# Kernel optimization log

Hardware: AMD Instinct MI355X
Metric: run time of the kernel (lower is better)

Reference implementation:

```python
import jax, jax.numpy as jnp
import numpy as np

EPS = 1e-5

def conv1x1(x, w, b):
    # x: [B,C,H,W], w: [O,C], b: [O]
    return jnp.einsum('bchw,oc->bohw', x, w) + b[None, :, None, None]

def batchnorm(x, gamma, beta):
    # training-mode BN: biased batch statistics over (N,H,W)
    mean = jnp.mean(x, axis=(0, 2, 3), keepdims=True)
    var = jnp.var(x, axis=(0, 2, 3), keepdims=True)
    inv = jax.lax.rsqrt(var + EPS)
    return (x - mean) * inv * gamma[None, :, None, None] + beta[None, :, None, None]

def setup_inputs() -> dict:
    key = jax.random.key(0)
    ks = jax.random.split(key, 20)
    B, H, W = 32, 480, 640
    d = {
        'x1': jax.random.normal(ks[0], (B, 3, H, W), dtype=jnp.float32),
        'w1': jax.random.normal(ks[1], (3, 3), dtype=jnp.float32) * 0.3,
        'b1': jax.random.normal(ks[2], (3,), dtype=jnp.float32) * 0.1,
        'g2': jnp.ones((3,), dtype=jnp.float32),
        'be2': jnp.zeros((3,), dtype=jnp.float32),
        'w3': jax.random.normal(ks[3], (8, 3), dtype=jnp.float32) * 0.3,
        'b3': jax.random.normal(ks[4], (8,), dtype=jnp.float32) * 0.1,
        'w4': jax.random.normal(ks[5], (8, 8), dtype=jnp.float32) * 0.2,
        'b4': jax.random.normal(ks[6], (8,), dtype=jnp.float32) * 0.1,
        'g5': jnp.ones((8,), dtype=jnp.float32),
        'be5': jnp.zeros((8,), dtype=jnp.float32),
        'w6': jax.random.normal(ks[7], (8, 8), dtype=jnp.float32) * 0.2,
        'b6': jax.random.normal(ks[8], (8,), dtype=jnp.float32) * 0.1,
        'w7': jax.random.normal(ks[9], (8, 8), dtype=jnp.float32) * 0.2,
        'b7': jax.random.normal(ks[10], (8,), dtype=jnp.float32) * 0.1,
        'w8': jax.random.normal(ks[11], (8, 8), dtype=jnp.float32) * 0.2,
        'b8': jax.random.normal(ks[12], (8,), dtype=jnp.float32) * 0.1,
    }
    return d

def reference(x1, w1, b1, g2, be2, w3, b3, w4, b4, g5, be5, w6, b6, w7, b7, w8, b8):
    v1 = conv1x1(x1, w1, b1)        # [B,3,H,W]
    v2 = batchnorm(v1, g2, be2)     # [B,3,H,W]
    v3 = conv1x1(v2, w3, b3)        # [B,8,H,W]
    v4 = conv1x1(v3, w4, b4)
    v5 = batchnorm(v4, g5, be5)
    v6 = conv1x1(v5, w6, b6)
    v7 = conv1x1(v6, w7, b7)
    v8 = conv1x1(v7, w8, b8)
    return v8
```

## Files before the change

kernel.cpp:

```cpp
#include <hip/hip_runtime.h>
#include <math.h>

#define HWD   (480*640)
#define HW4   (HWD/4)
#define BATCH 32
#define NPIXD ((double)BATCH*(double)HWD)
#define NPIX4 (BATCH*HW4)
#define RBLK  1024
#define BPI   32
#define ISTRIDE (BPI*256)
#define BN_EPS 1e-5

typedef float f32x4 __attribute__((ext_vector_type(4)));

__global__ __launch_bounds__(256) void k_reduce(const float* __restrict__ x,
                                                double* __restrict__ partials) {
    const int b   = blockIdx.x >> 5;
    const int blk = blockIdx.x & 31;
    const float4* xb = (const float4*)x + (long long)b*(3*HW4);

    float s0=0.f,s1=0.f,s2=0.f,s00=0.f,s01=0.f,s02=0.f,s11=0.f,s12=0.f,s22=0.f;
    for (int s = blk*256 + threadIdx.x; s < HW4; s += ISTRIDE) {
        const float4 a = xb[s];
        const float4 c = xb[s + HW4];
        const float4 e = xb[s + 2*HW4];
        float X0,X1,X2;
        X0=a.x; X1=c.x; X2=e.x;
        s0+=X0; s1+=X1; s2+=X2;
        s00=fmaf(X0,X0,s00); s01=fmaf(X0,X1,s01); s02=fmaf(X0,X2,s02);
        s11=fmaf(X1,X1,s11); s12=fmaf(X1,X2,s12); s22=fmaf(X2,X2,s22);
        X0=a.y; X1=c.y; X2=e.y;
        s0+=X0; s1+=X1; s2+=X2;
        s00=fmaf(X0,X0,s00); s01=fmaf(X0,X1,s01); s02=fmaf(X0,X2,s02);
        s11=fmaf(X1,X1,s11); s12=fmaf(X1,X2,s12); s22=fmaf(X2,X2,s22);
        X0=a.z; X1=c.z; X2=e.z;
        s0+=X0; s1+=X1; s2+=X2;
        s00=fmaf(X0,X0,s00); s01=fmaf(X0,X1,s01); s02=fmaf(X0,X2,s02);
        s11=fmaf(X1,X1,s11); s12=fmaf(X1,X2,s12); s22=fmaf(X2,X2,s22);
        X0=a.w; X1=c.w; X2=e.w;
        s0+=X0; s1+=X1; s2+=X2;
        s00=fmaf(X0,X0,s00); s01=fmaf(X0,X1,s01); s02=fmaf(X0,X2,s02);
        s11=fmaf(X1,X1,s11); s12=fmaf(X1,X2,s12); s22=fmaf(X2,X2,s22);
    }
    double v[9] = {(double)s0,(double)s1,(double)s2,(double)s00,(double)s01,
                   (double)s02,(double)s11,(double)s12,(double)s22};
    #pragma unroll
    for (int off = 32; off > 0; off >>= 1) {
        #pragma unroll
        for (int q = 0; q < 9; ++q) v[q] += __shfl_down(v[q], off, 64);
    }
    __shared__ double lds[4][9];
    const int lane = threadIdx.x & 63;
    const int wid  = threadIdx.x >> 6;
    if (lane == 0) {
        #pragma unroll
        for (int q = 0; q < 9; ++q) lds[wid][q] = v[q];
    }
    __syncthreads();
    if (threadIdx.x < 9) {
        partials[(long long)blockIdx.x*9 + threadIdx.x] =
            lds[0][threadIdx.x] + lds[1][threadIdx.x] + lds[2][threadIdx.x] + lds[3][threadIdx.x];
    }
}

__device__ void affine8(const float* __restrict__ w, const float* __restrict__ bias,
                        double A[8][3], double cc[8]) {
    double T[8][3], tc[8];
    for (int o = 0; o < 8; ++o) {
        double t0=0,t1=0,t2=0,tb=0;
        for (int c = 0; c < 8; ++c) {
            const double wv = (double)w[o*8+c];
            t0 += wv*A[c][0]; t1 += wv*A[c][1]; t2 += wv*A[c][2]; tb += wv*cc[c];
        }
        T[o][0]=t0; T[o][1]=t1; T[o][2]=t2; tc[o]=tb + (double)bias[o];
    }
    for (int o = 0; o < 8; ++o) { A[o][0]=T[o][0]; A[o][1]=T[o][1]; A[o][2]=T[o][2]; cc[o]=tc[o]; }
}

__device__ void bn8(int rows, const double m[3], const double C[3][3],
                    const float* __restrict__ g, const float* __restrict__ be,
                    double A[8][3], double cc[8]) {
    for (int o = 0; o < rows; ++o) {
        const double mu = A[o][0]*m[0] + A[o][1]*m[1] + A[o][2]*m[2] + cc[o];
        double var = 0;
        for (int i = 0; i < 3; ++i)
            for (int j = 0; j < 3; ++j)
                var += A[o][i]*A[o][j]*C[i][j];
        const double inv = 1.0 / sqrt(var + BN_EPS);
        const double sc  = inv * (double)g[o];
        A[o][0]*=sc; A[o][1]*=sc; A[o][2]*=sc;
        cc[o] = (cc[o]-mu)*sc + (double)be[o];
    }
}

__global__ __launch_bounds__(256) void k_apply2(const float* __restrict__ x,
        const double* __restrict__ partials,
        const float* __restrict__ w1, const float* __restrict__ b1,
        const float* __restrict__ g2, const float* __restrict__ be2,
        const float* __restrict__ w3, const float* __restrict__ b3,
        const float* __restrict__ w4, const float* __restrict__ b4,
        const float* __restrict__ g5, const float* __restrict__ be5,
        const float* __restrict__ w6, const float* __restrict__ b6,
        const float* __restrict__ w7, const float* __restrict__ b7,
        const float* __restrict__ w8, const float* __restrict__ b8,
        float* __restrict__ out) {
    __shared__ float4 MdS[8];
    {
        const int tid = threadIdx.x;
        double v[9] = {0,0,0,0,0,0,0,0,0};
        #pragma unroll
        for (int r = 0; r < 4; ++r) {
            const double* row = partials + (size_t)(r*256 + tid)*9;
            #pragma unroll
            for (int q = 0; q < 9; ++q) v[q] += row[q];
        }
        #pragma unroll
        for (int off = 32; off > 0; off >>= 1) {
            #pragma unroll
            for (int q = 0; q < 9; ++q) v[q] += __shfl_down(v[q], off, 64);
        }
        __shared__ double wsum[4][9];
        __shared__ double red[9];
        const int lane = tid & 63;
        const int wid  = tid >> 6;
        if (lane == 0) {
            #pragma unroll
            for (int q = 0; q < 9; ++q) wsum[wid][q] = v[q];
        }
        __syncthreads();
        if (tid < 9) red[tid] = wsum[0][tid] + wsum[1][tid] + wsum[2][tid] + wsum[3][tid];
        __syncthreads();

        if (tid == 0) {
            const double N = NPIXD;
            double m[3];
            for (int i = 0; i < 3; ++i) m[i] = red[i] / N;
            double S[3][3];
            S[0][0]=red[3]; S[0][1]=red[4]; S[0][2]=red[5];
            S[1][1]=red[6]; S[1][2]=red[7]; S[2][2]=red[8];
            S[1][0]=S[0][1]; S[2][0]=S[0][2]; S[2][1]=S[1][2];
            double C[3][3];
            for (int i = 0; i < 3; ++i)
                for (int j = 0; j < 3; ++j)
                    C[i][j] = S[i][j]/N - m[i]*m[j];

            double A[8][3], cc[8];
            for (int o = 0; o < 3; ++o) {
                A[o][0]=(double)w1[o*3+0]; A[o][1]=(double)w1[o*3+1]; A[o][2]=(double)w1[o*3+2];
                cc[o]=(double)b1[o];
            }
            bn8(3, m, C, g2, be2, A, cc);
            {
                double T[8][3], tc[8];
                for (int o = 0; o < 8; ++o) {
                    double t0=0,t1=0,t2=0,tb=0;
                    for (int c = 0; c < 3; ++c) {
                        const double wv = (double)w3[o*3+c];
                        t0 += wv*A[c][0]; t1 += wv*A[c][1]; t2 += wv*A[c][2]; tb += wv*cc[c];
                    }
                    T[o][0]=t0; T[o][1]=t1; T[o][2]=t2; tc[o]=tb + (double)b3[o];
                }
                for (int o = 0; o < 8; ++o) { A[o][0]=T[o][0]; A[o][1]=T[o][1]; A[o][2]=T[o][2]; cc[o]=tc[o]; }
            }
            affine8(w4, b4, A, cc);
            bn8(8, m, C, g5, be5, A, cc);
            affine8(w6, b6, A, cc);
            affine8(w7, b7, A, cc);
            affine8(w8, b8, A, cc);
            for (int o = 0; o < 8; ++o)
                MdS[o] = make_float4((float)A[o][0], (float)A[o][1], (float)A[o][2], (float)cc[o]);
        }
        __syncthreads();
    }

    const int b   = blockIdx.x >> 5;
    const int blk = blockIdx.x & 31;
    const float4* xb = (const float4*)x + (long long)b*(3*HW4);
    f32x4* ob = (f32x4*)out + (long long)b*(8*HW4);
    float4 M[8];
    #pragma unroll
    for (int o = 0; o < 8; ++o) M[o] = MdS[o];

    for (int s = blk*256 + threadIdx.x; s < HW4; s += ISTRIDE) {
        const float4 x0 = xb[s];
        const float4 x1 = xb[s + HW4];
        const float4 x2 = xb[s + 2*HW4];
        #pragma unroll
        for (int o = 0; o < 8; ++o) {
            const float4 mr = M[o];
            f32x4 r;
            r.x = fmaf(mr.x, x0.x, fmaf(mr.y, x1.x, fmaf(mr.z, x2.x, mr.w)));
            r.y = fmaf(mr.x, x0.y, fmaf(mr.y, x1.y, fmaf(mr.z, x2.y, mr.w)));
            r.z = fmaf(mr.x, x0.z, fmaf(mr.y, x1.z, fmaf(mr.z, x2.z, mr.w)));
            r.w = fmaf(mr.x, x0.w, fmaf(mr.y, x1.w, fmaf(mr.z, x2.w, mr.w)));
            __builtin_nontemporal_store(r, ob + (long long)o*HW4 + s);
        }
    }
}

extern "C" void kernel_launch(void* const* d_in, const int* in_sizes, int n_in,
                              void* d_out, int out_size, void* d_ws, size_t ws_size,
                              hipStream_t stream) {
    const float* x  = (const float*)d_in[0];
    const float* w1 = (const float*)d_in[1];
    const float* b1 = (const float*)d_in[2];
    const float* g2 = (const float*)d_in[3];
    const float* be2= (const float*)d_in[4];
    const float* w3 = (const float*)d_in[5];
    const float* b3 = (const float*)d_in[6];
    const float* w4 = (const float*)d_in[7];
    const float* b4 = (const float*)d_in[8];
    const float* g5 = (const float*)d_in[9];
    const float* be5= (const float*)d_in[10];
    const float* w6 = (const float*)d_in[11];
    const float* b6 = (const float*)d_in[12];
    const float* w7 = (const float*)d_in[13];
    const float* b7 = (const float*)d_in[14];
    const float* w8 = (const float*)d_in[15];
    const float* b8 = (const float*)d_in[16];

    double* partials = (double*)d_ws;
    float*  out      = (float*)d_out;

    k_reduce<<<RBLK, 256, 0, stream>>>(x, partials);
    k_apply2<<<RBLK, 256, 0, stream>>>(x, partials,
        w1,b1,g2,be2,w3,b3,w4,b4,g5,be5,w6,b6,w7,b7,w8,b8, out);
}
```

Baseline: 103.0 us.

## Fuse stats reduction and apply into one cooperative kernel with register-cached input

Merges the statistics-reduction and apply kernels into one cooperative kernel. Each thread loads its slice of x once, keeps it in registers across a grid-wide sync, and reuses it for the output pass, so x is no longer read twice from global memory. In exchange it adds a grid barrier, needs all 256 large blocks to be co-resident, and raises register pressure, which lowers occupancy.

Result: slower. 189.5 us (+84.0%).

```diff
diff --git a/kernel.cpp b/kernel.cpp
--- a/kernel.cpp
+++ b/kernel.cpp
@@ -1,67 +1,22 @@
 #include <hip/hip_runtime.h>
+#include <hip/hip_cooperative_groups.h>
 #include <math.h>
+
+namespace cg = cooperative_groups;
 
 #define HWD   (480*640)
 #define HW4   (HWD/4)
 #define BATCH 32
 #define NPIXD ((double)BATCH*(double)HWD)
-#define NPIX4 (BATCH*HW4)
-#define RBLK  1024
-#define BPI   32
-#define ISTRIDE (BPI*256)
+#define GRID  256
+#define TPB   1024
+#define BPI   8
+#define PPB   (HW4/BPI)
+#define KFULL 9
+#define KTAIL (PPB - KFULL*TPB)
 #define BN_EPS 1e-5
 
 typedef float f32x4 __attribute__((ext_vector_type(4)));
-
-__global__ __launch_bounds__(256) void k_reduce(const float* __restrict__ x,
-                                                double* __restrict__ partials) {
-    const int b   = blockIdx.x >> 5;
-    const int blk = blockIdx.x & 31;
-    const float4* xb = (const float4*)x + (long long)b*(3*HW4);
-
-    float s0=0.f,s1=0.f,s2=0.f,s00=0.f,s01=0.f,s02=0.f,s11=0.f,s12=0.f,s22=0.f;
-    for (int s = blk*256 + threadIdx.x; s < HW4; s += ISTRIDE) {
-        const float4 a = xb[s];
-        const float4 c = xb[s + HW4];
-        const float4 e = xb[s + 2*HW4];
-        float X0,X1,X2;
-        X0=a.x; X1=c.x; X2=e.x;
-        s0+=X0; s1+=X1; s2+=X2;
-        s00=fmaf(X0,X0,s00); s01=fmaf(X0,X1,s01); s02=fmaf(X0,X2,s02);
-        s11=fmaf(X1,X1,s11); s12=fmaf(X1,X2,s12); s22=fmaf(X2,X2,s22);
-        X0=a.y; X1=c.y; X2=e.y;
-        s0+=X0; s1+=X1; s2+=X2;
-        s00=fmaf(X0,X0,s00); s01=fmaf(X0,X1,s01); s02=fmaf(X0,X2,s02);
-        s11=fmaf(X1,X1,s11); s12=fmaf(X1,X2,s12); s22=fmaf(X2,X2,s22);
-        X0=a.z; X1=c.z; X2=e.z;
-        s0+=X0; s1+=X1; s2+=X2;
-        s00=fmaf(X0,X0,s00); s01=fmaf(X0,X1,s01); s02=fmaf(X0,X2,s02);
-        s11=fmaf(X1,X1,s11); s12=fmaf(X1,X2,s12); s22=fmaf(X2,X2,s22);
-        X0=a.w; X1=c.w; X2=e.w;
-        s0+=X0; s1+=X1; s2+=X2;
-        s00=fmaf(X0,X0,s00); s01=fmaf(X0,X1,s01); s02=fmaf(X0,X2,s02);
-        s11=fmaf(X1,X1,s11); s12=fmaf(X1,X2,s12); s22=fmaf(X2,X2,s22);
-    }
-    double v[9] = {(double)s0,(double)s1,(double)s2,(double)s00,(double)s01,
-                   (double)s02,(double)s11,(double)s12,(double)s22};
-    #pragma unroll
-    for (int off = 32; off > 0; off >>= 1) {
-        #pragma unroll
-        for (int q = 0; q < 9; ++q) v[q] += __shfl_down(v[q], off, 64);
-    }
-    __shared__ double lds[4][9];
-    const int lane = threadIdx.x & 63;
-    const int wid  = threadIdx.x >> 6;
-    if (lane == 0) {
-        #pragma unroll
-        for (int q = 0; q < 9; ++q) lds[wid][q] = v[q];
-    }
-    __syncthreads();
-    if (threadIdx.x < 9) {
-        partials[(long long)blockIdx.x*9 + threadIdx.x] =
-            lds[0][threadIdx.x] + lds[1][threadIdx.x] + lds[2][threadIdx.x] + lds[3][threadIdx.x];
-    }
-}
 
 __device__ void affine8(const float* __restrict__ w, const float* __restrict__ bias,
                         double A[8][3], double cc[8]) {
@@ -93,8 +48,8 @@
     }
 }
 
-__global__ __launch_bounds__(256) void k_apply2(const float* __restrict__ x,
-        const double* __restrict__ partials,
+__global__ __launch_bounds__(TPB, 4) void k_fused(const float* __restrict__ x,
+        double* __restrict__ partials,
         const float* __restrict__ w1, const float* __restrict__ b1,
         const float* __restrict__ g2, const float* __restrict__ be2,
         const float* __restrict__ w3, const float* __restrict__ b3,
@@ -104,23 +59,54 @@
         const float* __restrict__ w7, const float* __restrict__ b7,
         const float* __restrict__ w8, const float* __restrict__ b8,
         float* __restrict__ out) {
+    const int tid = threadIdx.x;
+    const int b   = blockIdx.x >> 3;
+    const int blk = blockIdx.x & 7;
+    const float4* xb = (const float4*)x + (long long)b*(3*HW4);
+    const int start = blk*PPB;
+
+    __shared__ double wsum[16][9];
+    __shared__ double red[9];
     __shared__ float4 MdS[8];
+
+    float4 X[10][3];
+    float s0=0.f,s1=0.f,s2=0.f,s00=0.f,s01=0.f,s02=0.f,s11=0.f,s12=0.f,s22=0.f;
+    #pragma unroll
+    for (int k = 0; k < 10; ++k) {
+        const int p = start + k*TPB + tid;
+        float4 a, c, e;
+        if (k < KFULL || tid < KTAIL) {
+            a = xb[p]; c = xb[p + HW4]; e = xb[p + 2*HW4];
+        } else {
+            a = make_float4(0.f,0.f,0.f,0.f); c = a; e = a;
+        }
+        X[k][0] = a; X[k][1] = c; X[k][2] = e;
+        float X0,X1,X2;
+        X0=a.x; X1=c.x; X2=e.x;
+        s0+=X0; s1+=X1; s2+=X2;
+        s00=fmaf(X0,X0,s00); s01=fmaf(X0,X1,s01); s02=fmaf(X0,X2,s02);
+        s11=fmaf(X1,X1,s11); s12=fmaf(X1,X2,s12); s22=fmaf(X2,X2,s22);
+        X0=a.y; X1=c.y; X2=e.y;
+        s0+=X0; s1+=X1; s2+=X2;
+        s00=fmaf(X0,X0,s00); s01=fmaf(X0,X1,s01); s02=fmaf(X0,X2,s02);
+        s11=fmaf(X1,X1,s11); s12=fmaf(X1,X2,s12); s22=fmaf(X2,X2,s22);
+        X0=a.z; X1=c.z; X2=e.z;
+        s0+=X0; s1+=X1; s2+=X2;
+        s00=fmaf(X0,X0,s00); s01=fmaf(X0,X1,s01); s02=fmaf(X0,X2,s02);
+        s11=fmaf(X1,X1,s11); s12=fmaf(X1,X2,s12); s22=fmaf(X2,X2,s22);
+        X0=a.w; X1=c.w; X2=e.w;
+        s0+=X0; s1+=X1; s2+=X2;
+        s00=fmaf(X0,X0,s00); s01=fmaf(X0,X1,s01); s02=fmaf(X0,X2,s02);
+        s11=fmaf(X1,X1,s11); s12=fmaf(X1,X2,s12); s22=fmaf(X2,X2,s22);
+    }
     {
-        const int tid = threadIdx.x;
-        double v[9] = {0,0,0,0,0,0,0,0,0};
-        #pragma unroll
-        for (int r = 0; r < 4; ++r) {
-            const double* row = partials + (size_t)(r*256 + tid)*9;
-            #pragma unroll
-            for (int q = 0; q < 9; ++q) v[q] += row[q];
-        }
+        double v[9] = {(double)s0,(double)s1,(double)s2,(double)s00,(double)s01,
+                       (double)s02,(double)s11,(double)s12,(double)s22};
         #pragma unroll
         for (int off = 32; off > 0; off >>= 1) {
             #pragma unroll
             for (int q = 0; q < 9; ++q) v[q] += __shfl_down(v[q], off, 64);
         }
-        __shared__ double wsum[4][9];
-        __shared__ double red[9];
         const int lane = tid & 63;
         const int wid  = tid >> 6;
         if (lane == 0) {
@@ -128,72 +114,99 @@
             for (int q = 0; q < 9; ++q) wsum[wid][q] = v[q];
         }
         __syncthreads();
-        if (tid < 9) red[tid] = wsum[0][tid] + wsum[1][tid] + wsum[2][tid] + wsum[3][tid];
-        __syncthreads();
-
-        if (tid == 0) {
-            const double N = NPIXD;
-            double m[3];
-            for (int i = 0; i < 3; ++i) m[i] = red[i] / N;
-            double S[3][3];
-            S[0][0]=red[3]; S[0][1]=red[4]; S[0][2]=red[5];
-            S[1][1]=red[6]; S[1][2]=red[7]; S[2][2]=red[8];
-            S[1][0]=S[0][1]; S[2][0]=S[0][2]; S[2][1]=S[1][2];
-            double C[3][3];
-            for (int i = 0; i < 3; ++i)
-                for (int j = 0; j < 3; ++j)
-                    C[i][j] = S[i][j]/N - m[i]*m[j];
-
-            double A[8][3], cc[8];
-            for (int o = 0; o < 3; ++o) {
-                A[o][0]=(double)w1[o*3+0]; A[o][1]=(double)w1[o*3+1]; A[o][2]=(double)w1[o*3+2];
-                cc[o]=(double)b1[o];
+        if (tid < 9) {
+            double acc = 0.0;
+            #pragma unroll
+            for (int w = 0; w < 16; ++w) acc += wsum[w][tid];
+            partials[(long long)blockIdx.x*9 + tid] = acc;
+        }
+    }
+
+    cg::this_grid().sync();
+
+    if (tid < 256) {
+        double v[9];
+        #pragma unroll
+        for (int q = 0; q < 9; ++q) v[q] = partials[(long long)tid*9 + q];
+        #pragma unroll
+        for (int off = 32; off > 0; off >>= 1) {
+            #pragma unroll
+            for (int q = 0; q < 9; ++q) v[q] += __shfl_down(v[q], off, 64);
+        }
+        const int lane = tid & 63;
+        const int wid  = tid >> 6;
+        if (lane == 0) {
+            #pragma unroll
+            for (int q = 0; q < 9; ++q) wsum[wid][q] = v[q];
+        }
+    }
+    __syncthreads();
+    if (tid < 9) red[tid] = wsum[0][tid] + wsum[1][tid] + wsum[2][tid] + wsum[3][tid];
+    __syncthreads();
+
+    if (tid == 0) {
+        const double N = NPIXD;
+        double m[3];
+        for (int i = 0; i < 3; ++i) m[i] = red[i] / N;
+        double S[3][3];
+        S[0][0]=red[3]; S[0][1]=red[4]; S[0][2]=red[5];
+        S[1][1]=red[6]; S[1][2]=red[7]; S[2][2]=red[8];
+        S[1][0]=S[0][1]; S[2][0]=S[0][2]; S[2][1]=S[1][2];
+        double C[3][3];
+        for (int i = 0; i < 3; ++i)
+            for (int j = 0; j < 3; ++j)
+                C[i][j] = S[i][j]/N - m[i]*m[j];
+
+        double A[8][3], cc[8];
+        for (int o = 0; o < 3; ++o) {
+            A[o][0]=(double)w1[o*3+0]; A[o][1]=(double)w1[o*3+1]; A[o][2]=(double)w1[o*3+2];
+            cc[o]=(double)b1[o];
+        }
+        bn8(3, m, C, g2, be2, A, cc);
+        {
+            double T[8][3], tc[8];
+            for (int o = 0; o < 8; ++o) {
+                double t0=0,t1=0,t2=0,tb=0;
+                for (int c = 0; c < 3; ++c) {
+                    const double wv = (double)w3[o*3+c];
+                    t0 += wv*A[c][0]; t1 += wv*A[c][1]; t2 += wv*A[c][2]; tb += wv*cc[c];
+                }
+                T[o][0]=t0; T[o][1]=t1; T[o][2]=t2; tc[o]=tb + (double)b3[o];
             }
-            bn8(3, m, C, g2, be2, A, cc);
-            {
-                double T[8][3], tc[8];
-                for (int o = 0; o < 8; ++o) {
-                    double t0=0,t1=0,t2=0,tb=0;
-                    for (int c = 0; c < 3; ++c) {
-                        const double wv = (double)w3[o*3+c];
-                        t0 += wv*A[c][0]; t1 += wv*A[c][1]; t2 += wv*A[c][2]; tb += wv*cc[c];
-                    }
-                    T[o][0]=t0; T[o][1]=t1; T[o][2]=t2; tc[o]=tb + (double)b3[o];
-                }
-                for (int o = 0; o < 8; ++o) { A[o][0]=T[o][0]; A[o][1]=T[o][1]; A[o][2]=T[o][2]; cc[o]=tc[o]; }
-            }
-            affine8(w4, b4, A, cc);
-            bn8(8, m, C, g5, be5, A, cc);
-            affine8(w6, b6, A, cc);
-            affine8(w7, b7, A, cc);
-            affine8(w8, b8, A, cc);
-            for (int o = 0; o < 8; ++o)
-                MdS[o] = make_float4((float)A[o][0], (float)A[o][1], (float)A[o][2], (float)cc[o]);
-        }
-        __syncthreads();
-    }
-
-    const int b   = blockIdx.x >> 5;
-    const int blk = blockIdx.x & 31;
-    const float4* xb = (const float4*)x + (long long)b*(3*HW4);
+            for (int o = 0; o < 8; ++o) { A[o][0]=T[o][0]; A[o][1]=T[o][1]; A[o][2]=T[o][2]; cc[o]=tc[o]; }
+        }
+        affine8(w4, b4, A, cc);
+        bn8(8, m, C, g5, be5, A, cc);
+        affine8(w6, b6, A, cc);
+        affine8(w7, b7, A, cc);
+        affine8(w8, b8, A, cc);
+        for (int o = 0; o < 8; ++o)
+            MdS[o] = make_float4((float)A[o][0], (float)A[o][1], (float)A[o][2], (float)cc[o]);
+    }
+    __syncthreads();
+
     f32x4* ob = (f32x4*)out + (long long)b*(8*HW4);
     float4 M[8];
     #pragma unroll
     for (int o = 0; o < 8; ++o) M[o] = MdS[o];
 
-    for (int s = blk*256 + threadIdx.x; s < HW4; s += ISTRIDE) {
-        const float4 x0 = xb[s];
-        const float4 x1 = xb[s + HW4];
-        const float4 x2 = xb[s + 2*HW4];
-        #pragma unroll
-        for (int o = 0; o < 8; ++o) {
-            const float4 mr = M[o];
-            f32x4 r;
-            r.x = fmaf(mr.x, x0.x, fmaf(mr.y, x1.x, fmaf(mr.z, x2.x, mr.w)));
-            r.y = fmaf(mr.x, x0.y, fmaf(mr.y, x1.y, fmaf(mr.z, x2.y, mr.w)));
-            r.z = fmaf(mr.x, x0.z, fmaf(mr.y, x1.z, fmaf(mr.z, x2.z, mr.w)));
-            r.w = fmaf(mr.x, x0.w, fmaf(mr.y, x1.w, fmaf(mr.z, x2.w, mr.w)));
-            __builtin_nontemporal_store(r, ob + (long long)o*HW4 + s);
+    #pragma unroll
+    for (int k = 0; k < 10; ++k) {
+        if (k < KFULL || tid < KTAIL) {
+            const int p = start + k*TPB + tid;
+            const float4 x0 = X[k][0];
+            const float4 x1 = X[k][1];
+            const float4 x2 = X[k][2];
+            #pragma unroll
+            for (int o = 0; o < 8; ++o) {
+                const float4 mr = M[o];
+                f32x4 r;
+                r.x = fmaf(mr.x, x0.x, fmaf(mr.y, x1.x, fmaf(mr.z, x2.x, mr.w)));
+                r.y = fmaf(mr.x, x0.y, fmaf(mr.y, x1.y, fmaf(mr.z, x2.y, mr.w)));
+                r.z = fmaf(mr.x, x0.z, fmaf(mr.y, x1.z, fmaf(mr.z, x2.z, mr.w)));
+                r.w = fmaf(mr.x, x0.w, fmaf(mr.y, x1.w, fmaf(mr.z, x2.w, mr.w)));
+                __builtin_nontemporal_store(r, ob + (long long)o*HW4 + p);
+            }
         }
     }
 }
@@ -222,7 +235,14 @@
     double* partials = (double*)d_ws;
     float*  out      = (float*)d_out;
 
-    k_reduce<<<RBLK, 256, 0, stream>>>(x, partials);
-    k_apply2<<<RBLK, 256, 0, stream>>>(x, partials,
-        w1,b1,g2,be2,w3,b3,w4,b4,g5,be5,w6,b6,w7,b7,w8,b8, out);
-}
+    void* args[] = {
+        (void*)&x, (void*)&partials,
+        (void*)&w1, (void*)&b1, (void*)&g2, (void*)&be2,
+        (void*)&w3, (void*)&b3, (void*)&w4, (void*)&b4,
+        (void*)&g5, (void*)&be5, (void*)&w6, (void*)&b6,
+        (void*)&w7, (void*)&b7, (void*)&w8, (void*)&b8,
+        (void*)&out
+    };
+    hipLaunchCooperativeKernel((const void*)k_fused, dim3(GRID), dim3(TPB),
+                               args, 0, stream);
+}
```
